# Performance work log

Hardware: AMD Instinct MI355X
Metric: run time of the kernel (lower is better)

Reference implementation:

```python
import jax, jax.numpy as jnp
import numpy as np

B, T, HID = 2, 2048, 1024
H, D = 16, 64
ROPE = 32
GIDX = (2, 3, 4, 5)
MASK_VAL = -1e9


def setup_inputs() -> dict:
    key = jax.random.key(0)
    ks = jax.random.split(key, 5)
    x = jax.random.normal(ks[0], (B, T, HID), jnp.float32)
    mask = jnp.triu(jnp.ones((T, T), jnp.bool_), 1)  # True above diagonal -> masked (causal)
    qkv_w = jax.random.normal(ks[1], (3 * H * D, HID), jnp.float32) * (1.0 / np.sqrt(HID))
    qkv_b = jax.random.normal(ks[2], (3 * H * D,), jnp.float32) * 0.02
    out_w = jax.random.normal(ks[3], (HID, H * D), jnp.float32) * (1.0 / np.sqrt(H * D))
    out_b = jax.random.normal(ks[4], (HID,), jnp.float32) * 0.02
    return {"x": x, "mask": mask, "qkv_w": qkv_w, "qkv_b": qkv_b, "out_w": out_w, "out_b": out_b}


def _rope_tables(t):
    inv_freq = 1.0 / (10000.0 ** (jnp.arange(0, ROPE, 2, dtype=jnp.float32) / ROPE))
    freqs = jnp.arange(t, dtype=jnp.float32)[:, None] * inv_freq[None, :]  # [T, ROPE/2]
    return jnp.cos(freqs), jnp.sin(freqs)


def _apply_rotary(x, cos, sin):
    # x: [B,H,T,D]; rotate first ROPE dims as interleaved pairs
    xr = x[..., :ROPE].reshape(*x.shape[:-1], ROPE // 2, 2)
    x1, x2 = xr[..., 0], xr[..., 1]
    rot = jnp.stack([x1 * cos - x2 * sin, x1 * sin + x2 * cos], axis=-1).reshape(*x.shape[:-1], ROPE)
    return jnp.concatenate([rot, x[..., ROPE:]], axis=-1)


def reference(x, mask, qkv_w, qkv_b, out_w, out_b):
    b, t, _ = x.shape
    qkv = x @ qkv_w.T + qkv_b                      # [B,T,3*H*D]
    q, k, v = jnp.split(qkv, 3, axis=-1)
    q, k, v = [y.reshape(b, t, H, D).transpose(0, 2, 1, 3) for y in (q, k, v)]  # [B,H,T,D]
    cos, sin = _rope_tables(t)                      # [T, ROPE/2] broadcast over B,H
    q = _apply_rotary(q, cos, sin)
    k = _apply_rotary(k, cos, sin)
    scale = 1.0 / np.sqrt(D)
    # local dense causal attention
    scores = jnp.einsum('bhqd,bhkd->bhqk', q, k) * scale
    scores = jnp.where(mask, MASK_VAL, scores)
    out_local = jnp.einsum('bhqk,bhkd->bhqd', jax.nn.softmax(scores, axis=-1), v)
    # global token pass with its own causal overlay
    gidx = jnp.array(GIDX)
    gq = q[:, :, gidx]                              # [B,H,G,D]
    gs = jnp.einsum('bhgd,bhkd->bhgk', gq, k) * scale
    gmask = jnp.arange(t)[None, :] > gidx[:, None]  # [G,T]: col > row -> masked
    gs = jnp.where(gmask, MASK_VAL, gs)
    gout = jnp.einsum('bhgk,bhkd->bhgd', jax.nn.softmax(gs, axis=-1), v)
    out = out_local.at[:, :, gidx].set(gout)
    attn_out = out.transpose(0, 2, 1, 3).reshape(b, t, H * D)
    return attn_out @ out_w.T + out_b
```

## Files before the change

### kernel.cpp

```cpp
#include <hip/hip_runtime.h>
#include <math.h>

typedef unsigned short u16;
typedef unsigned int u32;
typedef __attribute__((ext_vector_type(4))) float f32x4;
typedef __attribute__((ext_vector_type(8))) short bf16x8;

#define B_ 2
#define T_ 2048
#define H_ 16
#define HID 1024
#define NQKV 3072
#define M_ 4096

__device__ __forceinline__ u16 f2bf(float f) {
  union { float f; unsigned u; } v; v.f = f;
  unsigned r = v.u + 0x7FFFu + ((v.u >> 16) & 1u);
  return (u16)(r >> 16);
}
__device__ __forceinline__ float bf2f(u16 u) {
  union { unsigned u; float f; } v; v.u = ((unsigned)u) << 16; return v.f;
}

__device__ __forceinline__ void gload16(const void* g, void* l) {
  __builtin_amdgcn_global_load_lds((const __attribute__((address_space(1))) void*)g,
                                   (__attribute__((address_space(3))) void*)l, 16, 0, 0);
}

__global__ void cvt_bf16(const float* __restrict__ in, u16* __restrict__ out, int n4) {
  int i = blockIdx.x * blockDim.x + threadIdx.x;
  if (i >= n4) return;
  float4 v = ((const float4*)in)[i];
  uint2 o;
  o.x = (unsigned)f2bf(v.x) | ((unsigned)f2bf(v.y) << 16);
  o.y = (unsigned)f2bf(v.z) | ((unsigned)f2bf(v.w) << 16);
  ((uint2*)out)[i] = o;
}

__global__ void rope_tab(float* __restrict__ tab) {
  int i = blockIdx.x * 256 + threadIdx.x;
  int tpos = i >> 4, f = i & 15;
  float ang = (float)tpos * exp2f(-(float)f * 0.83048202372184058696f);
  float s, c;
  sincosf(ang, &s, &c);
  tab[i * 2] = c;
  tab[i * 2 + 1] = s;
}

template<int OUT_BF16>
__global__ __launch_bounds__(256) void gemm_nt(const u16* __restrict__ A,
    const u16* __restrict__ Bt, const float* __restrict__ bias,
    void* __restrict__ outp, int N, int K)
{
  __shared__ u16 lsA[128 * 32];
  __shared__ u16 lsB[128 * 32];
  const int t = threadIdx.x;
  const int l = t & 63, w = t >> 6;
  const int wm = (w >> 1) * 64, wn = (w & 1) * 64;
  const int lr = l & 15, lg = l >> 4;
  const long bm = (long)blockIdx.y * 128, bn = (long)blockIdx.x * 128;

  f32x4 acc[4][4];
#pragma unroll
  for (int i = 0; i < 4; i++)
#pragma unroll
    for (int j = 0; j < 4; j++) acc[i][j] = (f32x4){0.f, 0.f, 0.f, 0.f};

  const int srow = l >> 2, sko = (l & 3) * 8;
  const u16* Ab = A + (bm + srow) * (long)K + sko;
  const u16* Bb = Bt + (bn + srow) * (long)K + sko;
  const int s0 = 2 * w, s1 = 2 * w + 1;

  for (int k0 = 0; k0 < K; k0 += 32) {
    if (k0) __syncthreads();
    gload16(Ab + (long)(s0 * 16) * K + k0, &lsA[s0 * 512]);
    gload16(Ab + (long)(s1 * 16) * K + k0, &lsA[s1 * 512]);
    gload16(Bb + (long)(s0 * 16) * K + k0, &lsB[s0 * 512]);
    gload16(Bb + (long)(s1 * 16) * K + k0, &lsB[s1 * 512]);
    __syncthreads();
    bf16x8 af[4], bfv[4];
#pragma unroll
    for (int mi = 0; mi < 4; mi++)
      af[mi] = *(const bf16x8*)&lsA[(wm + mi * 16 + lr) * 32 + lg * 8];
#pragma unroll
    for (int ni = 0; ni < 4; ni++)
      bfv[ni] = *(const bf16x8*)&lsB[(wn + ni * 16 + lr) * 32 + lg * 8];
#pragma unroll
    for (int mi = 0; mi < 4; mi++)
#pragma unroll
      for (int ni = 0; ni < 4; ni++)
        acc[mi][ni] = __builtin_amdgcn_mfma_f32_16x16x32_bf16(af[mi], bfv[ni], acc[mi][ni], 0, 0, 0);
  }
#pragma unroll
  for (int mi = 0; mi < 4; mi++)
#pragma unroll
    for (int ni = 0; ni < 4; ni++) {
      long row = bm + wm + mi * 16 + lg * 4;
      long col = bn + wn + ni * 16 + lr;
      float bv = bias[col];
#pragma unroll
      for (int r = 0; r < 4; r++) {
        float v = acc[mi][ni][r] + bv;
        if (OUT_BF16) ((u16*)outp)[(row + r) * (long)N + col] = f2bf(v);
        else          ((float*)outp)[(row + r) * (long)N + col] = v;
      }
    }
}

__global__ void rope_qk(const u16* __restrict__ qkv, const float* __restrict__ tab,
                        u16* __restrict__ Q, u16* __restrict__ K) {
  int idx = blockIdx.x * 256 + threadIdx.x;
  int h = idx & 15;
  int m = idx >> 4;
  int tpos = m & (T_ - 1);
  int b = m >> 11;
  const u16* qr = qkv + (long)m * NQKV + h * 64;
  alignas(16) u16 qv[64];
  alignas(16) u16 kv[64];
#pragma unroll
  for (int c = 0; c < 8; c++) {
    *(int4*)&qv[c * 8] = *(const int4*)&qr[c * 8];
    *(int4*)&kv[c * 8] = *(const int4*)&qr[1024 + c * 8];
  }
#pragma unroll
  for (int i = 0; i < 16; i++) {
    float c = tab[(tpos * 16 + i) * 2];
    float s = tab[(tpos * 16 + i) * 2 + 1];
    float q1 = bf2f(qv[2 * i]), q2 = bf2f(qv[2 * i + 1]);
    qv[2 * i]     = f2bf((q1 * c - q2 * s) * 0.125f);
    qv[2 * i + 1] = f2bf((q1 * s + q2 * c) * 0.125f);
    float k1 = bf2f(kv[2 * i]), k2 = bf2f(kv[2 * i + 1]);
    kv[2 * i]     = f2bf(k1 * c - k2 * s);
    kv[2 * i + 1] = f2bf(k1 * s + k2 * c);
  }
#pragma unroll
  for (int j = 32; j < 64; j++) qv[j] = f2bf(bf2f(qv[j]) * 0.125f);
  long ob = ((long)(b * 16 + h) * T_ + tpos) * 64;
#pragma unroll
  for (int c = 0; c < 8; c++) {
    *(int4*)&Q[ob + c * 8] = *(int4*)&qv[c * 8];
    *(int4*)&K[ob + c * 8] = *(int4*)&kv[c * 8];
  }
}

__global__ __launch_bounds__(256) void v_trans(const u16* __restrict__ qkv, u16* __restrict__ Vt) {
  int tt = blockIdx.x, bh = blockIdx.y;
  int b = bh >> 4, h = bh & 15;
  __shared__ u16 ls[64 * 72];
  int t = threadIdx.x;
  for (int c = t; c < 512; c += 256) {
    int row = c >> 3, off = (c & 7) * 8;
    *(int4*)&ls[row * 72 + off] =
        *(const int4*)&qkv[((long)(b * T_ + tt * 64 + row)) * NQKV + 2048 + h * 64 + off];
  }
  __syncthreads();
  for (int c = t; c < 512; c += 256) {
    int d = c >> 3, toff = (c & 7) * 8;
    alignas(16) u16 tmp[8];
#pragma unroll
    for (int j = 0; j < 8; j++) tmp[j] = ls[(toff + j) * 72 + d];
    *(int4*)&Vt[((long)(bh * 64 + d)) * T_ + tt * 64 + toff] = *(int4*)tmp;
  }
}

__global__ __launch_bounds__(256, 4) void fattn(const u16* __restrict__ Q, const u16* __restrict__ Kp,
                                                const u16* __restrict__ V, u16* __restrict__ O) {
  const int id = blockIdx.x;
  const int qt = 31 - (id >> 5);
  const int bh = id & 31;
  __shared__ u16 lsK[64 * 64];
  __shared__ u16 lsV[64 * 64];
  __shared__ u32 lsP[4 * 16 * 36];
  const int t = threadIdx.x, l = t & 63, w = t >> 6;
  const int lr = l & 15, lg = l >> 4;
  const u16* Qb = Q + (long)bh * T_ * 64;
  const u16* Kb = Kp + (long)bh * T_ * 64;
  const u16* Vb = V + (long)bh * 64 * T_;
  u32* lsPw = lsP + w * 576;

  bf16x8 aq[2];
#pragma unroll
  for (int ks = 0; ks < 2; ks++)
    aq[ks] = *(const bf16x8*)&Qb[((long)(qt * 64 + w * 16 + lr)) * 64 + ks * 32 + lg * 8];

  f32x4 o[4];
#pragma unroll
  for (int di = 0; di < 4; di++) o[di] = (f32x4){0.f, 0.f, 0.f, 0.f};
  float mrow = -1e30f, lrow = 0.f;

  const int srow = l >> 3;
  const int scx = ((l & 7) ^ srow) * 8;

  for (int kt = 0; kt <= qt; kt++) {
    if (kt) __syncthreads();
    const u16* kp = Kb + kt * 4096;
    const u16* vp = Vb + kt * 64;
    gload16(kp + (long)(16 * w + srow) * 64 + scx,       &lsK[(2 * w) * 512]);
    gload16(kp + (long)(16 * w + 8 + srow) * 64 + scx,   &lsK[(2 * w + 1) * 512]);
    gload16(vp + (long)(16 * w + srow) * T_ + scx,       &lsV[(2 * w) * 512]);
    gload16(vp + (long)(16 * w + 8 + srow) * T_ + scx,   &lsV[(2 * w + 1) * 512]);
    __syncthreads();

    f32x4 s[4];
#pragma unroll
    for (int ji = 0; ji < 4; ji++) s[ji] = (f32x4){0.f, 0.f, 0.f, 0.f};
#pragma unroll
    for (int ks = 0; ks < 2; ks++)
#pragma unroll
      for (int ji = 0; ji < 4; ji++) {
        int row = ji * 16 + lr;
        bf16x8 kf = *(const bf16x8*)&lsK[row * 64 + ((ks * 32 + lg * 8) ^ ((row & 7) * 8))];
        s[ji] = __builtin_amdgcn_mfma_f32_16x16x32_bf16(kf, aq[ks], s[ji], 0, 0, 0);
      }

    if (kt == qt) {
      int qloc = w * 16 + lr;
#pragma unroll
      for (int ji = 0; ji < 4; ji++)
#pragma unroll
        for (int r = 0; r < 4; r++)
          if (ji * 16 + lg * 4 + r > qloc) s[ji][r] = -1e30f;
    }

    float mx = s[0][0];
#pragma unroll
    for (int ji = 0; ji < 4; ji++)
#pragma unroll
      for (int r = 0; r < 4; r++) mx = fmaxf(mx, s[ji][r]);
    mx = fmaxf(mx, __shfl_xor(mx, 16, 64));
    mx = fmaxf(mx, __shfl_xor(mx, 32, 64));
    bool grow = mx > mrow;
    float newm = fmaxf(mrow, mx);
    float rs = 0.f;
    u32 pd[8];
#pragma unroll
    for (int ji = 0; ji < 4; ji++)
#pragma unroll
      for (int hh = 0; hh < 2; hh++) {
        float p0 = __expf(s[ji][2 * hh] - newm);
        float p1 = __expf(s[ji][2 * hh + 1] - newm);
        rs += p0 + p1;
        pd[ji * 2 + hh] = (u32)f2bf(p0) | ((u32)f2bf(p1) << 16);
      }
    rs += __shfl_xor(rs, 16, 64);
    rs += __shfl_xor(rs, 32, 64);
    if (__any(grow)) {
      float sf = __expf(mrow - newm);
      lrow = lrow * sf + rs;
#pragma unroll
      for (int r = 0; r < 4; r++) {
        float sfb = __shfl(sf, lg * 4 + r, 64);
#pragma unroll
        for (int di = 0; di < 4; di++) o[di][r] *= sfb;
      }
    } else {
      lrow += rs;
    }
    mrow = newm;

#pragma unroll
    for (int ji = 0; ji < 4; ji++)
      *(uint2*)&lsPw[lr * 36 + ji * 8 + lg * 2] = make_uint2(pd[2 * ji], pd[2 * ji + 1]);
#pragma unroll
    for (int js = 0; js < 2; js++) {
      bf16x8 pa = *(const bf16x8*)&lsPw[lr * 36 + js * 16 + lg * 4];
#pragma unroll
      for (int di = 0; di < 4; di++) {
        int drow = di * 16 + lr;
        bf16x8 vb = *(const bf16x8*)&lsV[drow * 64 + ((js * 32 + lg * 8) ^ ((drow & 7) * 8))];
        o[di] = __builtin_amdgcn_mfma_f32_16x16x32_bf16(pa, vb, o[di], 0, 0, 0);
      }
    }
  }

  const int b = bh >> 4, h = bh & 15;
  float inv = 1.f / lrow;
#pragma unroll
  for (int r = 0; r < 4; r++) {
    float invb = __shfl(inv, lg * 4 + r, 64);
#pragma unroll
    for (int di = 0; di < 4; di++) {
      long rowt = (long)(b * T_ + qt * 64 + w * 16 + lg * 4 + r);
      O[rowt * 1024 + h * 64 + di * 16 + lr] = f2bf(o[di][r] * invb);
    }
  }
}

extern "C" void kernel_launch(void* const* d_in, const int* in_sizes, int n_in,
                              void* d_out, int out_size, void* d_ws, size_t ws_size,
                              hipStream_t stream) {
  (void)in_sizes; (void)n_in; (void)out_size; (void)ws_size;
  const float* x     = (const float*)d_in[0];
  const float* qkv_w = (const float*)d_in[2];
  const float* qkv_b = (const float*)d_in[3];
  const float* out_w = (const float*)d_in[4];
  const float* out_b = (const float*)d_in[5];
  char* ws = (char*)d_ws;
  size_t off = 0;
  auto alloc = [&](size_t n) { void* p = ws + off; off += (n + 255) & ~(size_t)255; return p; };
  u16*   xb    = (u16*)alloc((size_t)M_ * HID * 2);
  u16*   wqkv  = (u16*)alloc((size_t)NQKV * HID * 2);
  u16*   wout  = (u16*)alloc((size_t)HID * HID * 2);
  u16*   qkvb  = (u16*)alloc((size_t)M_ * NQKV * 2);
  u16*   Qb    = (u16*)alloc((size_t)M_ * HID * 2);
  u16*   Kb    = (u16*)alloc((size_t)M_ * HID * 2);
  u16*   Vtb   = (u16*)alloc((size_t)M_ * HID * 2);
  u16*   attnb = (u16*)alloc((size_t)M_ * HID * 2);
  float* tab   = (float*)alloc((size_t)T_ * 16 * 2 * 4);

  rope_tab<<<T_ * 16 / 256, 256, 0, stream>>>(tab);
  cvt_bf16<<<(M_ * HID / 4 + 255) / 256, 256, 0, stream>>>(x, xb, M_ * HID / 4);
  cvt_bf16<<<(NQKV * HID / 4 + 255) / 256, 256, 0, stream>>>(qkv_w, wqkv, NQKV * HID / 4);
  cvt_bf16<<<(HID * HID / 4 + 255) / 256, 256, 0, stream>>>(out_w, wout, HID * HID / 4);
  gemm_nt<1><<<dim3(NQKV / 128, M_ / 128), 256, 0, stream>>>(xb, wqkv, qkv_b, qkvb, NQKV, HID);
  rope_qk<<<(B_ * T_ * H_) / 256, 256, 0, stream>>>(qkvb, tab, Qb, Kb);
  v_trans<<<dim3(T_ / 64, B_ * H_), 256, 0, stream>>>(qkvb, Vtb);
  fattn<<<1024, 256, 0, stream>>>(Qb, Kb, Vtb, attnb);
  gemm_nt<0><<<dim3(HID / 128, M_ / 128), 256, 0, stream>>>(attnb, wout, out_b, (float*)d_out, HID, HID);
}
```

Measured before the change: 223.4 us.

## Double-buffer GEMM and attention loads, fuse prep kernels, use exp2 lazy-rescale softmax

Merges the rope table and three fp32-to-bf16 conversions into one prep launch, and merges RoPE and the V transpose into one post-QKV kernel, cutting launch count. The GEMM and flash-attention loops now double-buffer LDS so the next tile's global load overlaps MFMA work, with s_setprio raised around the MFMA blocks. Softmax folds log2(e) into the Q scale and uses exp2, a packed bf16 convert, and a lazy rescale that only updates the running max when it grows by more than 8. The output projection uses 64-row tiles to launch more blocks. The extra LDS buffers may lower occupancy, and the lazy max threshold lets unnormalised exponentials grow larger before rescaling.

```diff
diff --git a/kernel.cpp b/kernel.cpp
--- a/kernel.cpp
+++ b/kernel.cpp
@@ -12,6 +12,7 @@
 #define HID 1024
 #define NQKV 3072
 #define M_ 4096
+#define SCALE_Q 0.18033688011112042f
 
 __device__ __forceinline__ u16 f2bf(float f) {
   union { float f; unsigned u; } v; v.f = f;
@@ -21,15 +22,39 @@
 __device__ __forceinline__ float bf2f(u16 u) {
   union { unsigned u; float f; } v; v.u = ((unsigned)u) << 16; return v.f;
 }
+__device__ __forceinline__ u32 cvt_pk_bf16(float lo, float hi) {
+  u32 r;
+  asm("v_cvt_pk_bf16_f32 %0, %1, %2" : "=v"(r) : "v"(lo), "v"(hi));
+  return r;
+}
+__device__ __forceinline__ float fexp2(float x) { return __builtin_amdgcn_exp2f(x); }
 
 __device__ __forceinline__ void gload16(const void* g, void* l) {
   __builtin_amdgcn_global_load_lds((const __attribute__((address_space(1))) void*)g,
                                    (__attribute__((address_space(3))) void*)l, 16, 0, 0);
 }
 
-__global__ void cvt_bf16(const float* __restrict__ in, u16* __restrict__ out, int n4) {
-  int i = blockIdx.x * blockDim.x + threadIdx.x;
-  if (i >= n4) return;
+__global__ void prep(const float* __restrict__ x, const float* __restrict__ qkv_w,
+                     const float* __restrict__ out_w, u16* __restrict__ xb,
+                     u16* __restrict__ wqkv, u16* __restrict__ wout, float* __restrict__ tab) {
+  int bid = blockIdx.x;
+  if (bid < 128) {
+    int i = bid * 256 + threadIdx.x;
+    int tpos = i >> 4, f = i & 15;
+    float ang = (float)tpos * exp2f(-(float)f * 0.83048202372184058696f);
+    float s, c;
+    sincosf(ang, &s, &c);
+    tab[i * 2] = c;
+    tab[i * 2 + 1] = s;
+    return;
+  }
+  bid -= 128;
+  const float* in;
+  u16* out;
+  if (bid < 4096) { in = x; out = xb; }
+  else if (bid < 7168) { bid -= 4096; in = qkv_w; out = wqkv; }
+  else { bid -= 7168; in = out_w; out = wout; }
+  int i = bid * 256 + threadIdx.x;
   float4 v = ((const float4*)in)[i];
   uint2 o;
   o.x = (unsigned)f2bf(v.x) | ((unsigned)f2bf(v.y) << 16);
@@ -37,64 +62,67 @@
   ((uint2*)out)[i] = o;
 }
 
-__global__ void rope_tab(float* __restrict__ tab) {
-  int i = blockIdx.x * 256 + threadIdx.x;
-  int tpos = i >> 4, f = i & 15;
-  float ang = (float)tpos * exp2f(-(float)f * 0.83048202372184058696f);
-  float s, c;
-  sincosf(ang, &s, &c);
-  tab[i * 2] = c;
-  tab[i * 2 + 1] = s;
-}
-
-template<int OUT_BF16>
+template<int BM, int WROWS, int OUT_BF16>
 __global__ __launch_bounds__(256) void gemm_nt(const u16* __restrict__ A,
     const u16* __restrict__ Bt, const float* __restrict__ bias,
     void* __restrict__ outp, int N, int K)
 {
-  __shared__ u16 lsA[128 * 32];
-  __shared__ u16 lsB[128 * 32];
+  constexpr int WCOLS = 4 / WROWS;
+  constexpr int MI = BM / WROWS / 16;
+  constexpr int NI = 128 / WCOLS / 16;
+  __shared__ u16 lsA[2][BM * 32];
+  __shared__ u16 lsB[2][128 * 32];
   const int t = threadIdx.x;
   const int l = t & 63, w = t >> 6;
-  const int wm = (w >> 1) * 64, wn = (w & 1) * 64;
+  const int wm = (w / WCOLS) * (BM / WROWS);
+  const int wn = (w % WCOLS) * (128 / WCOLS);
   const int lr = l & 15, lg = l >> 4;
-  const long bm = (long)blockIdx.y * 128, bn = (long)blockIdx.x * 128;
-
-  f32x4 acc[4][4];
-#pragma unroll
-  for (int i = 0; i < 4; i++)
-#pragma unroll
-    for (int j = 0; j < 4; j++) acc[i][j] = (f32x4){0.f, 0.f, 0.f, 0.f};
+  const long bm = (long)blockIdx.y * BM, bn = (long)blockIdx.x * 128;
+
+  f32x4 acc[MI][NI];
+#pragma unroll
+  for (int i = 0; i < MI; i++)
+#pragma unroll
+    for (int j = 0; j < NI; j++) acc[i][j] = (f32x4){0.f, 0.f, 0.f, 0.f};
 
   const int srow = l >> 2, sko = (l & 3) * 8;
   const u16* Ab = A + (bm + srow) * (long)K + sko;
   const u16* Bb = Bt + (bn + srow) * (long)K + sko;
-  const int s0 = 2 * w, s1 = 2 * w + 1;
-
+
+  auto stage = [&](int buf, int k0) {
+    gload16(Ab + (long)(w * 16) * K + k0, &lsA[buf][w * 512]);
+    if constexpr (BM == 128)
+      gload16(Ab + (long)((w + 4) * 16) * K + k0, &lsA[buf][(w + 4) * 512]);
+    gload16(Bb + (long)(w * 16) * K + k0, &lsB[buf][w * 512]);
+    gload16(Bb + (long)((w + 4) * 16) * K + k0, &lsB[buf][(w + 4) * 512]);
+  };
+
+  stage(0, 0);
+  __syncthreads();
+  int cur = 0;
   for (int k0 = 0; k0 < K; k0 += 32) {
-    if (k0) __syncthreads();
-    gload16(Ab + (long)(s0 * 16) * K + k0, &lsA[s0 * 512]);
-    gload16(Ab + (long)(s1 * 16) * K + k0, &lsA[s1 * 512]);
-    gload16(Bb + (long)(s0 * 16) * K + k0, &lsB[s0 * 512]);
-    gload16(Bb + (long)(s1 * 16) * K + k0, &lsB[s1 * 512]);
+    if (k0 + 32 < K) stage(cur ^ 1, k0 + 32);
+    bf16x8 af[MI], bfv[NI];
+#pragma unroll
+    for (int mi = 0; mi < MI; mi++)
+      af[mi] = *(const bf16x8*)&lsA[cur][(wm + mi * 16 + lr) * 32 + lg * 8];
+#pragma unroll
+    for (int ni = 0; ni < NI; ni++)
+      bfv[ni] = *(const bf16x8*)&lsB[cur][(wn + ni * 16 + lr) * 32 + lg * 8];
+    __builtin_amdgcn_s_setprio(1);
+#pragma unroll
+    for (int mi = 0; mi < MI; mi++)
+#pragma unroll
+      for (int ni = 0; ni < NI; ni++)
+        acc[mi][ni] = __builtin_amdgcn_mfma_f32_16x16x32_bf16(af[mi], bfv[ni], acc[mi][ni], 0, 0, 0);
+    __builtin_amdgcn_s_setprio(0);
     __syncthreads();
-    bf16x8 af[4], bfv[4];
-#pragma unroll
-    for (int mi = 0; mi < 4; mi++)
-      af[mi] = *(const bf16x8*)&lsA[(wm + mi * 16 + lr) * 32 + lg * 8];
-#pragma unroll
-    for (int ni = 0; ni < 4; ni++)
-      bfv[ni] = *(const bf16x8*)&lsB[(wn + ni * 16 + lr) * 32 + lg * 8];
-#pragma unroll
-    for (int mi = 0; mi < 4; mi++)
-#pragma unroll
-      for (int ni = 0; ni < 4; ni++)
-        acc[mi][ni] = __builtin_amdgcn_mfma_f32_16x16x32_bf16(af[mi], bfv[ni], acc[mi][ni], 0, 0, 0);
-  }
-#pragma unroll
-  for (int mi = 0; mi < 4; mi++)
-#pragma unroll
-    for (int ni = 0; ni < 4; ni++) {
+    cur ^= 1;
+  }
+#pragma unroll
+  for (int mi = 0; mi < MI; mi++)
+#pragma unroll
+    for (int ni = 0; ni < NI; ni++) {
       long row = bm + wm + mi * 16 + lg * 4;
       long col = bn + wn + ni * 16 + lr;
       float bv = bias[col];
@@ -107,59 +135,62 @@
     }
 }
 
-__global__ void rope_qk(const u16* __restrict__ qkv, const float* __restrict__ tab,
-                        u16* __restrict__ Q, u16* __restrict__ K) {
-  int idx = blockIdx.x * 256 + threadIdx.x;
-  int h = idx & 15;
-  int m = idx >> 4;
-  int tpos = m & (T_ - 1);
-  int b = m >> 11;
-  const u16* qr = qkv + (long)m * NQKV + h * 64;
-  alignas(16) u16 qv[64];
-  alignas(16) u16 kv[64];
-#pragma unroll
-  for (int c = 0; c < 8; c++) {
-    *(int4*)&qv[c * 8] = *(const int4*)&qr[c * 8];
-    *(int4*)&kv[c * 8] = *(const int4*)&qr[1024 + c * 8];
-  }
-#pragma unroll
-  for (int i = 0; i < 16; i++) {
-    float c = tab[(tpos * 16 + i) * 2];
-    float s = tab[(tpos * 16 + i) * 2 + 1];
-    float q1 = bf2f(qv[2 * i]), q2 = bf2f(qv[2 * i + 1]);
-    qv[2 * i]     = f2bf((q1 * c - q2 * s) * 0.125f);
-    qv[2 * i + 1] = f2bf((q1 * s + q2 * c) * 0.125f);
-    float k1 = bf2f(kv[2 * i]), k2 = bf2f(kv[2 * i + 1]);
-    kv[2 * i]     = f2bf(k1 * c - k2 * s);
-    kv[2 * i + 1] = f2bf(k1 * s + k2 * c);
-  }
-#pragma unroll
-  for (int j = 32; j < 64; j++) qv[j] = f2bf(bf2f(qv[j]) * 0.125f);
-  long ob = ((long)(b * 16 + h) * T_ + tpos) * 64;
-#pragma unroll
-  for (int c = 0; c < 8; c++) {
-    *(int4*)&Q[ob + c * 8] = *(int4*)&qv[c * 8];
-    *(int4*)&K[ob + c * 8] = *(int4*)&kv[c * 8];
-  }
-}
-
-__global__ __launch_bounds__(256) void v_trans(const u16* __restrict__ qkv, u16* __restrict__ Vt) {
-  int tt = blockIdx.x, bh = blockIdx.y;
-  int b = bh >> 4, h = bh & 15;
+__global__ __launch_bounds__(256) void post_qkv(const u16* __restrict__ qkv,
+    const float* __restrict__ tab, u16* __restrict__ Q, u16* __restrict__ K,
+    u16* __restrict__ Vt) {
   __shared__ u16 ls[64 * 72];
-  int t = threadIdx.x;
-  for (int c = t; c < 512; c += 256) {
-    int row = c >> 3, off = (c & 7) * 8;
-    *(int4*)&ls[row * 72 + off] =
-        *(const int4*)&qkv[((long)(b * T_ + tt * 64 + row)) * NQKV + 2048 + h * 64 + off];
-  }
-  __syncthreads();
-  for (int c = t; c < 512; c += 256) {
-    int d = c >> 3, toff = (c & 7) * 8;
-    alignas(16) u16 tmp[8];
-#pragma unroll
-    for (int j = 0; j < 8; j++) tmp[j] = ls[(toff + j) * 72 + d];
-    *(int4*)&Vt[((long)(bh * 64 + d)) * T_ + tt * 64 + toff] = *(int4*)tmp;
+  const int bid = blockIdx.x;
+  if (bid < 256) {
+    int idx = bid * 256 + threadIdx.x;
+    int h = idx & 15;
+    int m = idx >> 4;
+    int tpos = m & (T_ - 1);
+    int b = m >> 11;
+    const u16* qr = qkv + (long)m * NQKV + h * 64;
+    alignas(16) u16 qv[64];
+    alignas(16) u16 kv[64];
+#pragma unroll
+    for (int c = 0; c < 8; c++) {
+      *(int4*)&qv[c * 8] = *(const int4*)&qr[c * 8];
+      *(int4*)&kv[c * 8] = *(const int4*)&qr[1024 + c * 8];
+    }
+#pragma unroll
+    for (int i = 0; i < 16; i++) {
+      float c = tab[(tpos * 16 + i) * 2];
+      float s = tab[(tpos * 16 + i) * 2 + 1];
+      float q1 = bf2f(qv[2 * i]), q2 = bf2f(qv[2 * i + 1]);
+      qv[2 * i]     = f2bf((q1 * c - q2 * s) * SCALE_Q);
+      qv[2 * i + 1] = f2bf((q1 * s + q2 * c) * SCALE_Q);
+      float k1 = bf2f(kv[2 * i]), k2 = bf2f(kv[2 * i + 1]);
+      kv[2 * i]     = f2bf(k1 * c - k2 * s);
+      kv[2 * i + 1] = f2bf(k1 * s + k2 * c);
+    }
+#pragma unroll
+    for (int j = 32; j < 64; j++) qv[j] = f2bf(bf2f(qv[j]) * SCALE_Q);
+    long ob = ((long)(b * 16 + h) * T_ + tpos) * 64;
+#pragma unroll
+    for (int c = 0; c < 8; c++) {
+      *(int4*)&Q[ob + c * 8] = *(int4*)&qv[c * 8];
+      *(int4*)&K[ob + c * 8] = *(int4*)&kv[c * 8];
+    }
+  } else {
+    int id2 = bid - 256;
+    int tt = id2 & 31, bh = id2 >> 5;
+    int b = bh >> 4, h = bh & 15;
+    int t = threadIdx.x;
+    for (int c = t; c < 512; c += 256) {
+      int row = c >> 3, off = (c & 7) * 8;
+      *(int4*)&ls[row * 72 + off] =
+          *(const int4*)&qkv[((long)(b * T_ + tt * 64 + row)) * NQKV + 2048 + h * 64 + off];
+    }
+    __syncthreads();
+    for (int c = t; c < 512; c += 256) {
+      int d = c >> 3, toff = (c & 7) * 8;
+      alignas(16) u16 tmp[8];
+#pragma unroll
+      for (int j = 0; j < 8; j++) tmp[j] = ls[(toff + j) * 72 + d];
+      *(int4*)&Vt[((long)(bh * 64 + d)) * T_ + tt * 64 + toff] = *(int4*)tmp;
+    }
   }
 }
 
@@ -168,15 +199,15 @@
   const int id = blockIdx.x;
   const int qt = 31 - (id >> 5);
   const int bh = id & 31;
-  __shared__ u16 lsK[64 * 64];
-  __shared__ u16 lsV[64 * 64];
-  __shared__ u32 lsP[4 * 16 * 36];
+  __shared__ u16 lsK[2][64 * 64];
+  __shared__ u16 lsV[2][64 * 64];
+  __shared__ u32 lsP[4][16 * 36];
   const int t = threadIdx.x, l = t & 63, w = t >> 6;
   const int lr = l & 15, lg = l >> 4;
   const u16* Qb = Q + (long)bh * T_ * 64;
   const u16* Kb = Kp + (long)bh * T_ * 64;
   const u16* Vb = V + (long)bh * 64 * T_;
-  u32* lsPw = lsP + w * 576;
+  u32* lsPw = lsP[w];
 
   bf16x8 aq[2];
 #pragma unroll
@@ -190,28 +221,41 @@
 
   const int srow = l >> 3;
   const int scx = ((l & 7) ^ srow) * 8;
-
+  const long kgo0 = (long)(16 * w + srow) * 64 + scx;
+  const long kgo1 = (long)(16 * w + 8 + srow) * 64 + scx;
+  const long vgo0 = (long)(16 * w + srow) * T_ + scx;
+  const long vgo1 = (long)(16 * w + 8 + srow) * T_ + scx;
+
+  gload16(Kb + kgo0, &lsK[0][(2 * w) * 512]);
+  gload16(Kb + kgo1, &lsK[0][(2 * w + 1) * 512]);
+  gload16(Vb + vgo0, &lsV[0][(2 * w) * 512]);
+  gload16(Vb + vgo1, &lsV[0][(2 * w + 1) * 512]);
+  __syncthreads();
+
+  int cur = 0;
   for (int kt = 0; kt <= qt; kt++) {
-    if (kt) __syncthreads();
-    const u16* kp = Kb + kt * 4096;
-    const u16* vp = Vb + kt * 64;
-    gload16(kp + (long)(16 * w + srow) * 64 + scx,       &lsK[(2 * w) * 512]);
-    gload16(kp + (long)(16 * w + 8 + srow) * 64 + scx,   &lsK[(2 * w + 1) * 512]);
-    gload16(vp + (long)(16 * w + srow) * T_ + scx,       &lsV[(2 * w) * 512]);
-    gload16(vp + (long)(16 * w + 8 + srow) * T_ + scx,   &lsV[(2 * w + 1) * 512]);
-    __syncthreads();
+    if (kt < qt) {
+      const u16* kp = Kb + (kt + 1) * 4096;
+      const u16* vp = Vb + (kt + 1) * 64;
+      gload16(kp + kgo0, &lsK[cur ^ 1][(2 * w) * 512]);
+      gload16(kp + kgo1, &lsK[cur ^ 1][(2 * w + 1) * 512]);
+      gload16(vp + vgo0, &lsV[cur ^ 1][(2 * w) * 512]);
+      gload16(vp + vgo1, &lsV[cur ^ 1][(2 * w + 1) * 512]);
+    }
 
     f32x4 s[4];
 #pragma unroll
     for (int ji = 0; ji < 4; ji++) s[ji] = (f32x4){0.f, 0.f, 0.f, 0.f};
+    __builtin_amdgcn_s_setprio(1);
 #pragma unroll
     for (int ks = 0; ks < 2; ks++)
 #pragma unroll
       for (int ji = 0; ji < 4; ji++) {
         int row = ji * 16 + lr;
-        bf16x8 kf = *(const bf16x8*)&lsK[row * 64 + ((ks * 32 + lg * 8) ^ ((row & 7) * 8))];
+        bf16x8 kf = *(const bf16x8*)&lsK[cur][row * 64 + ((ks * 32 + lg * 8) ^ ((row & 7) * 8))];
         s[ji] = __builtin_amdgcn_mfma_f32_16x16x32_bf16(kf, aq[ks], s[ji], 0, 0, 0);
       }
+    __builtin_amdgcn_s_setprio(0);
 
     if (kt == qt) {
       int qloc = w * 16 + lr;
@@ -229,48 +273,53 @@
       for (int r = 0; r < 4; r++) mx = fmaxf(mx, s[ji][r]);
     mx = fmaxf(mx, __shfl_xor(mx, 16, 64));
     mx = fmaxf(mx, __shfl_xor(mx, 32, 64));
-    bool grow = mx > mrow;
-    float newm = fmaxf(mrow, mx);
+
+    if (__any(mx - mrow > 8.f)) {
+      float newm = fmaxf(mrow, mx);
+      float sf = fexp2(mrow - newm);
+      mrow = newm;
+      lrow *= sf;
+#pragma unroll
+      for (int r = 0; r < 4; r++) {
+        float sfb = __shfl(sf, lg * 4 + r, 64);
+#pragma unroll
+        for (int di = 0; di < 4; di++) o[di][r] *= sfb;
+      }
+    }
+
     float rs = 0.f;
     u32 pd[8];
 #pragma unroll
     for (int ji = 0; ji < 4; ji++)
 #pragma unroll
       for (int hh = 0; hh < 2; hh++) {
-        float p0 = __expf(s[ji][2 * hh] - newm);
-        float p1 = __expf(s[ji][2 * hh + 1] - newm);
+        float p0 = fexp2(s[ji][2 * hh] - mrow);
+        float p1 = fexp2(s[ji][2 * hh + 1] - mrow);
         rs += p0 + p1;
-        pd[ji * 2 + hh] = (u32)f2bf(p0) | ((u32)f2bf(p1) << 16);
+        pd[ji * 2 + hh] = cvt_pk_bf16(p0, p1);
       }
     rs += __shfl_xor(rs, 16, 64);
     rs += __shfl_xor(rs, 32, 64);
-    if (__any(grow)) {
-      float sf = __expf(mrow - newm);
-      lrow = lrow * sf + rs;
-#pragma unroll
-      for (int r = 0; r < 4; r++) {
-        float sfb = __shfl(sf, lg * 4 + r, 64);
-#pragma unroll
-        for (int di = 0; di < 4; di++) o[di][r] *= sfb;
-      }
-    } else {
-      lrow += rs;
-    }
-    mrow = newm;
+    lrow += rs;
 
 #pragma unroll
     for (int ji = 0; ji < 4; ji++)
       *(uint2*)&lsPw[lr * 36 + ji * 8 + lg * 2] = make_uint2(pd[2 * ji], pd[2 * ji + 1]);
+    __builtin_amdgcn_s_setprio(1);
 #pragma unroll
     for (int js = 0; js < 2; js++) {
       bf16x8 pa = *(const bf16x8*)&lsPw[lr * 36 + js * 16 + lg * 4];
 #pragma unroll
       for (int di = 0; di < 4; di++) {
         int drow = di * 16 + lr;
-        bf16x8 vb = *(const bf16x8*)&lsV[drow * 64 + ((js * 32 + lg * 8) ^ ((drow & 7) * 8))];
+        bf16x8 vb = *(const bf16x8*)&lsV[cur][drow * 64 + ((js * 32 + lg * 8) ^ ((drow & 7) * 8))];
         o[di] = __builtin_amdgcn_mfma_f32_16x16x32_bf16(pa, vb, o[di], 0, 0, 0);
       }
     }
+    __builtin_amdgcn_s_setprio(0);
+
+    if (kt < qt) __syncthreads();
+    cur ^= 1;
   }
 
   const int b = bh >> 4, h = bh & 15;
@@ -308,13 +357,9 @@
   u16*   attnb = (u16*)alloc((size_t)M_ * HID * 2);
   float* tab   = (float*)alloc((size_t)T_ * 16 * 2 * 4);
 
-  rope_tab<<<T_ * 16 / 256, 256, 0, stream>>>(tab);
-  cvt_bf16<<<(M_ * HID / 4 + 255) / 256, 256, 0, stream>>>(x, xb, M_ * HID / 4);
-  cvt_bf16<<<(NQKV * HID / 4 + 255) / 256, 256, 0, stream>>>(qkv_w, wqkv, NQKV * HID / 4);
-  cvt_bf16<<<(HID * HID / 4 + 255) / 256, 256, 0, stream>>>(out_w, wout, HID * HID / 4);
-  gemm_nt<1><<<dim3(NQKV / 128, M_ / 128), 256, 0, stream>>>(xb, wqkv, qkv_b, qkvb, NQKV, HID);
-  rope_qk<<<(B_ * T_ * H_) / 256, 256, 0, stream>>>(qkvb, tab, Qb, Kb);
-  v_trans<<<dim3(T_ / 64, B_ * H_), 256, 0, stream>>>(qkvb, Vtb);
+  prep<<<8320, 256, 0, stream>>>(x, qkv_w, out_w, xb, wqkv, wout, tab);
+  gemm_nt<128, 2, 1><<<dim3(NQKV / 128, M_ / 128), 256, 0, stream>>>(xb, wqkv, qkv_b, qkvb, NQKV, HID);
+  post_qkv<<<1280, 256, 0, stream>>>(qkvb, tab, Qb, Kb, Vtb);
   fattn<<<1024, 256, 0, stream>>>(Qb, Kb, Vtb, attnb);
-  gemm_nt<0><<<dim3(HID / 128, M_ / 128), 256, 0, stream>>>(attnb, wout, out_b, (float*)d_out, HID, HID);
-}
+  gemm_nt<64, 1, 0><<<dim3(HID / 128, M_ / 64), 256, 0, stream>>>(attnb, wout, out_b, (float*)d_out, HID, HID);
+}
```

After: 210.7 us. 1.06x faster.
